# Optimization experiments

Hardware: AMD Instinct MI355X
Metric: run time of the kernel (lower is better)

The kernel has to match this reference:

```python
import jax, jax.numpy as jnp
import numpy as np

N_VOX = (128, 128, 8)            # (X, Y, Z) voxels
D_BINS = 66                      # int((50 - 0) / 0.75)
DEPTH_RANGE = (0.0, 50.0)
IMG_H, IMG_W = 512.0, 1408.0     # img_pad_shape / img_shape (features are stride-16: 32x88)
PC_RANGE = (-51.2, -51.2, -5.0, 51.2, 51.2, 3.0)


def _make_points():
    # voxel-center anchors, laid out so reshape(n_voxels[::-1]+[-1]) = [Z,Y,X,C] (x fastest)
    nx, ny, nz = N_VOX
    x0, y0, z0, x1, y1, z1 = PC_RANGE
    xc = x0 + (np.arange(nx) + 0.5) * (x1 - x0) / nx
    yc = y0 + (np.arange(ny) + 0.5) * (y1 - y0) / ny
    zc = z0 + (np.arange(nz) + 0.5) * (z1 - z0) / nz
    zz, yy, xx = np.meshgrid(zc, yc, xc, indexing='ij')
    return np.stack([xx, yy, zz], -1).reshape(-1, 3).astype(np.float32)


def _make_proj(B, N):
    # realistic ori_lidar2img: pinhole K @ [R|t], six surround cameras 60 deg apart
    K = np.array([[560., 0., 704., 0.], [0., 560., 256., 0.],
                  [0., 0., 1., 0.], [0., 0., 0., 1.]], np.float64)
    mats = []
    for n in range(N):
        th = 2.0 * np.pi * n / N
        fwd = np.array([np.cos(th), np.sin(th), 0.0])
        right = np.array([np.sin(th), -np.cos(th), 0.0])
        down = np.array([0.0, 0.0, -1.0])
        Rt = np.eye(4)
        Rt[:3, :3] = np.stack([right, down, fwd])
        Rt[:3, 3] = [0.0, 0.2, 0.0]
        mats.append(K @ Rt)
    P = np.stack(mats).astype(np.float32)
    return np.broadcast_to(P, (B, N, 4, 4)).copy()


def setup_inputs() -> dict:
    key = jax.random.key(0)
    B, N, C, H, W = 1, 6, 64, 32, 88
    k1, k2, k3 = jax.random.split(key, 3)
    return {
        'x_fov': jax.random.normal(k1, (B, N, C, H, W), jnp.float32),
        'w_dn': jax.random.normal(k2, (C + D_BINS, C), jnp.float32) * 0.05,
        'b_dn': jax.random.normal(k3, (C + D_BINS,), jnp.float32) * 0.05,
        'points': jnp.asarray(_make_points()),
        'proj_mats': jnp.asarray(_make_proj(B, N)),
    }


def _trilinear(vol, gx, gy, gz):
    # vol: [C, D, H, W]; gx/gy/gz: [P] continuous indices along W/H/D
    # grid_sample(align_corners=False, padding_mode='zeros') semantics
    C, D, H, W = vol.shape
    x0f, y0f, z0f = jnp.floor(gx), jnp.floor(gy), jnp.floor(gz)
    tx, ty, tz = gx - x0f, gy - y0f, gz - z0f
    x0, y0, z0 = x0f.astype(jnp.int32), y0f.astype(jnp.int32), z0f.astype(jnp.int32)
    out = jnp.zeros((C, gx.shape[0]), vol.dtype)
    for dz, wz in ((0, 1.0 - tz), (1, tz)):
        for dy, wy in ((0, 1.0 - ty), (1, ty)):
            for dx, wx in ((0, 1.0 - tx), (1, tx)):
                xi, yi, zi = x0 + dx, y0 + dy, z0 + dz
                inb = ((xi >= 0) & (xi < W) & (yi >= 0) & (yi < H)
                       & (zi >= 0) & (zi < D))
                w = (wx * wy * wz) * inb.astype(vol.dtype)  # [P]
                corner = vol[:, jnp.clip(zi, 0, D - 1),
                             jnp.clip(yi, 0, H - 1),
                             jnp.clip(xi, 0, W - 1)]        # [C, P]
                out = out + corner * w
    return out.T  # [P, C]


def reference(x_fov, w_dn, b_dn, points, proj_mats):
    B, N, C, H, W = x_fov.shape
    nx, ny, nz = N_VOX
    dr0, dr1 = DEPTH_RANGE
    # 1x1 conv depth_net
    y = jnp.einsum('bnchw,oc->bnohw', x_fov, w_dn) + b_dn[None, None, :, None, None]
    depth = jax.nn.softmax(y[:, :, :D_BINS], axis=2)       # [B,N,D,H,W]
    feat = y[:, :, D_BINS:]                                # [B,N,C,H,W]
    # LSS outer product -> [B,N,C,D,H,W]
    vol = depth[:, :, None] * feat[:, :, :, None]
    # project voxel centers into each camera
    hom = jnp.concatenate([points, jnp.ones_like(points[:, :1])], -1)  # [P,4]
    pts = jnp.einsum('bnij,pj->bnpi', proj_mats, hom)      # [B,N,P,4]
    z = pts[..., 2]
    zs = jnp.where(jnp.abs(z) > 1e-3, z, 1e-3)
    u = pts[..., 0] / zs
    v = pts[..., 1] / zs
    valid = ((u >= 0) & (u < IMG_W) & (v >= 0) & (v < IMG_H)
             & (z > dr0) & (z < dr1))                      # [B,N,P]
    # normalized->index coords (align_corners=False): idx = norm01*size - 0.5
    gx = u / IMG_W * W - 0.5
    gy = v / IMG_H * H - 0.5
    gz = (z - dr0) / (dr1 - dr0) * D_BINS - 0.5
    P = points.shape[0]
    samp = jax.vmap(_trilinear)(vol.reshape(B * N, C, D_BINS, H, W),
                                gx.reshape(B * N, P),
                                gy.reshape(B * N, P),
                                gz.reshape(B * N, P))      # [B*N,P,C]
    samp = samp.reshape(B, N, P, C) * valid[..., None].astype(samp.dtype)
    counts = valid.astype(samp.dtype).sum(1)               # [B,P]
    ssum = samp.sum(1)                                     # [B,P,C]
    out = jnp.where(counts[..., None] > 0,
                    ssum / jnp.clip(counts, 1e-3, None)[..., None],
                    jnp.zeros_like(ssum))
    # [B,P,C] -> [B,Z,Y,X,C] -> [B,C,X,Y,Z]
    return out.reshape(B, nz, ny, nx, C).transpose(0, 4, 3, 2, 1)
```

## Files before the change

kernel.cpp:

```cpp
#include <hip/hip_runtime.h>
#include <math.h>

#define NCAM 6
#define CCH  64
#define DB   66
#define FH   32
#define FW   88
#define NX   128
#define NY   128
#define NZ   8
#define NPTS (NX*NY*NZ)
#define NPIX (NCAM*FH*FW)
#define PPC  (FH*FW)

#define TPX   32
#define DN_T  256
#define WS2   132
#define YSS   35
#define OFF_XS 0
#define OFF_WT 2048
#define OFF_YS 2048
#define OFF_BS 10496
#define LDS_F  10626

__global__ __launch_bounds__(DN_T) void depthnet_kernel(
    const float* __restrict__ x_fov, const float* __restrict__ w_dn,
    const float* __restrict__ b_dn, float* __restrict__ feat_t,
    float* __restrict__ depth_t)
{
    __shared__ float lds[LDS_F];
    float* xs = lds + OFF_XS;
    float* wT = lds + OFF_WT;
    float* ys = lds + OFF_YS;
    float* bs = lds + OFF_BS;

    const int t   = threadIdx.x;
    const int T   = blockIdx.x * TPX;
    const int cam = T / PPC;
    const int ph0 = T - cam * PPC;

    if (t < DB + CCH) bs[t] = b_dn[t];
    for (int i = t; i < (DB + CCH) * CCH; i += DN_T) {
        const int o = i >> 6, c = i & 63;
        wT[c * WS2 + o] = w_dn[i];
    }
    {
        const float* xb = x_fov + (size_t)cam * CCH * PPC + ph0;
        const int c = t >> 2;
        const int q = t & 3;
        #pragma unroll
        for (int h = 0; h < 2; ++h) {
            const float4 v = *(const float4*)(xb + c * PPC + h * 16 + q * 4);
            *(float4*)(xs + c * TPX + h * 16 + q * 4) = v;
        }
    }
    __syncthreads();

    const int pq = t & 3;
    const int oq = t >> 2;
    float acc[2][8];
    float acc2[2][8];
    #pragma unroll
    for (int a = 0; a < 2; ++a)
        #pragma unroll
        for (int p = 0; p < 8; ++p) { acc[a][p] = 0.f; acc2[a][p] = 0.f; }

    {
        const float* xr  = xs + pq * 8;
        const float* wr  = wT + oq * 2;
        const float* wr2 = wT + 128;
        #pragma unroll 4
        for (int c = 0; c < 64; ++c) {
            const float4 xa = *(const float4*)(xr + c * TPX);
            const float4 xb2 = *(const float4*)(xr + c * TPX + 4);
            const float2 wv = *(const float2*)(wr + c * WS2);
            const float xv[8] = {xa.x, xa.y, xa.z, xa.w, xb2.x, xb2.y, xb2.z, xb2.w};
            #pragma unroll
            for (int p = 0; p < 8; ++p) {
                acc[0][p] += wv.x * xv[p];
                acc[1][p] += wv.y * xv[p];
            }
            if (oq == 0) {
                const float2 w2 = *(const float2*)(wr2 + c * WS2);
                #pragma unroll
                for (int p = 0; p < 8; ++p) {
                    acc2[0][p] += w2.x * xv[p];
                    acc2[1][p] += w2.y * xv[p];
                }
            }
        }
    }
    __syncthreads();

    #pragma unroll
    for (int a = 0; a < 2; ++a) {
        const int o = 2 * oq + a;
        const float b = bs[o];
        #pragma unroll
        for (int p = 0; p < 8; ++p) ys[o * YSS + pq * 8 + p] = acc[a][p] + b;
    }
    if (oq == 0) {
        #pragma unroll
        for (int a = 0; a < 2; ++a) {
            const int o = 128 + a;
            const float b = bs[o];
            #pragma unroll
            for (int p = 0; p < 8; ++p) ys[o * YSS + pq * 8 + p] = acc2[a][p] + b;
        }
    }
    __syncthreads();

    {
        const int spx = t >> 3;
        const int r   = t & 7;
        float m = -1e30f;
        #pragma unroll
        for (int i = 0; i < 9; ++i) {
            const int o = r + 8 * i;
            if (o < DB) m = fmaxf(m, ys[o * YSS + spx]);
        }
        m = fmaxf(m, __shfl_xor(m, 1));
        m = fmaxf(m, __shfl_xor(m, 2));
        m = fmaxf(m, __shfl_xor(m, 4));
        float e[9];
        float ssum = 0.f;
        #pragma unroll
        for (int i = 0; i < 9; ++i) {
            const int o = r + 8 * i;
            const float v = (o < DB) ? expf(ys[o * YSS + spx] - m) : 0.f;
            e[i] = v;
            ssum += v;
        }
        ssum += __shfl_xor(ssum, 1);
        ssum += __shfl_xor(ssum, 2);
        ssum += __shfl_xor(ssum, 4);
        const float inv = 1.f / ssum;
        #pragma unroll
        for (int i = 0; i < 9; ++i) {
            const int o = r + 8 * i;
            if (o < DB) depth_t[(size_t)(T + spx) * DB + o] = e[i] * inv;
        }
    }

    for (int i = t; i < TPX * CCH; i += DN_T) {
        const int px = i >> 6, o = i & 63;
        feat_t[(size_t)T * CCH + i] = ys[(DB + o) * YSS + px];
    }
}

__global__ __launch_bounds__(256) void splat_kernel(
    const float* __restrict__ feat_t, const float* __restrict__ depth_t,
    const float* __restrict__ proj, float* __restrict__ out)
{
    __shared__ float trans[64 * 33];
    const int t    = threadIdx.x;
    const int w    = t >> 6;
    const int lane = t & 63;
    const int g    = lane >> 3;
    const int s    = lane & 7;
    const int gb   = lane & 56;
    const int ix   = blockIdx.x >> 5;
    const int iy0  = 4 * (blockIdx.x & 31);
    const int iy   = iy0 + w;

    const double DXY = 102.4 / 128.0;
    const float px = (float)(-51.2 + (ix + 0.5) * DXY);
    const float py = (float)(-51.2 + (iy + 0.5) * DXY);
    const float pz = (float)(-5.0 + (g + 0.5) * 1.0);

    float wcs_l[4] = {0.f, 0.f, 0.f, 0.f};
    int   pixc_l[4] = {0, 0, 0, 0};
    bool validm = false;
    if (s < NCAM) {
        const float* M = proj + s * 16;
        const float u4 = M[0] * px + M[1] * py + M[2]  * pz + M[3];
        const float v4 = M[4] * px + M[5] * py + M[6]  * pz + M[7];
        const float z  = M[8] * px + M[9] * py + M[10] * pz + M[11];
        const float zs = fabsf(z) > 0.001f ? z : 0.001f;
        const float u = u4 / zs;
        const float v = v4 / zs;
        validm = (u >= 0.f) && (u < 1408.f) && (v >= 0.f) && (v < 512.f) &&
                 (z > 0.f) && (z < 50.f);
        if (validm) {
            const float gx = u / 1408.0f * (float)FW - 0.5f;
            const float gy = v / 512.0f  * (float)FH - 0.5f;
            const float gz = z / 50.0f   * (float)DB - 0.5f;
            const float xf = floorf(gx), yf = floorf(gy), zf = floorf(gz);
            const float tx = gx - xf, ty = gy - yf, tz = gz - zf;
            const int x0 = (int)xf, y0 = (int)yf, z0 = (int)zf;

            const float wz0 = (z0 >= 0 && z0 < DB) ? (1.f - tz) : 0.f;
            const float wz1 = (z0 + 1 < DB) ? tz : 0.f;
            const int zi0 = min(max(z0, 0), DB - 1);
            const int zi1 = min(max(z0 + 1, 0), DB - 1);

            #pragma unroll
            for (int dy = 0; dy < 2; ++dy) {
                const int yi = y0 + dy;
                const bool yin = (yi >= 0) & (yi < FH);
                const int yic = min(max(yi, 0), FH - 1);
                const float wy = (dy ? ty : 1.f - ty) * (yin ? 1.f : 0.f);
                #pragma unroll
                for (int dx = 0; dx < 2; ++dx) {
                    const int xi = x0 + dx;
                    const bool xin = (xi >= 0) & (xi < FW);
                    const int xic = min(max(xi, 0), FW - 1);
                    const float wx = (dx ? tx : 1.f - tx) * (xin ? 1.f : 0.f);
                    pixc_l[2 * dy + dx] = (s * FH + yic) * FW + xic;
                    wcs_l[2 * dy + dx]  = wx * wy;
                }
            }
            #pragma unroll
            for (int k = 0; k < 4; ++k) {
                const float* dptr = depth_t + (size_t)pixc_l[k] * DB;
                wcs_l[k] *= wz0 * dptr[zi0] + wz1 * dptr[zi1];
            }
        }
    }
    const unsigned long long bal = __ballot(validm);
    const float cnt = (float)__popcll((bal >> (g * 8)) & 0x3Full);

    float acc[8];
    #pragma unroll
    for (int a = 0; a < 8; ++a) acc[a] = 0.f;

    for (int cam = 0; cam < NCAM; ++cam) {
        if ((bal >> (gb + cam)) & 1ull) {
            #pragma unroll
            for (int k = 0; k < 4; ++k) {
                const float wc  = __shfl(wcs_l[k], gb | cam);
                const int   pcx = __shfl(pixc_l[k], gb | cam);
                const float* fb = feat_t + (size_t)pcx * CCH + s * 4;
                const float4 fa = *(const float4*)(fb);
                const float4 fh = *(const float4*)(fb + 32);
                acc[0] += wc * fa.x; acc[1] += wc * fa.y;
                acc[2] += wc * fa.z; acc[3] += wc * fa.w;
                acc[4] += wc * fh.x; acc[5] += wc * fh.y;
                acc[6] += wc * fh.z; acc[7] += wc * fh.w;
            }
        }
    }

    const float invc = cnt > 0.f ? 1.f / cnt : 0.f;
    #pragma unroll
    for (int j = 0; j < 4; ++j) {
        trans[(4 * s + j) * 33 + w * 8 + g]      = acc[j]     * invc;
        trans[(32 + 4 * s + j) * 33 + w * 8 + g] = acc[4 + j] * invc;
    }
    __syncthreads();
    {
        const int idx = t & 31;
        const int cb  = t >> 5;
        const size_t obase = (size_t)ix * (NY * NZ) + iy0 * 8 + idx;
        #pragma unroll
        for (int i = 0; i < 8; ++i) {
            const int c = cb + 8 * i;
            out[(size_t)c * NPTS + obase] = trans[c * 33 + idx];
        }
    }
}

extern "C" void kernel_launch(void* const* d_in, const int* in_sizes, int n_in,
                              void* d_out, int out_size, void* d_ws, size_t ws_size,
                              hipStream_t stream) {
    const float* x_fov = (const float*)d_in[0];
    const float* w_dn  = (const float*)d_in[1];
    const float* b_dn  = (const float*)d_in[2];
    const float* proj  = (const float*)d_in[4];
    float* out = (float*)d_out;

    float* feat_t  = (float*)d_ws;
    float* depth_t = feat_t + (size_t)NPIX * CCH;

    depthnet_kernel<<<NPIX / TPX, DN_T, 0, stream>>>(x_fov, w_dn, b_dn, feat_t, depth_t);

    splat_kernel<<<(NX * NY) / 4, 256, 0, stream>>>(feat_t, depth_t, proj, out);
}
```

Baseline: 102.5 us.

## Use one-wave splat blocks with swizzled block order and direct stores

The splat kernel now launches one 64-thread block per (x,y) column instead of four columns per 256-thread block. Blocks are remapped with a swizzle, (L&7)*2048 + (L>>3), which spreads consecutive block IDs across distant columns, presumably to balance work across XCDs and CUs. The LDS transpose and barrier are gone, and each thread writes its outputs straight to global memory. The cost is less coalesced stores: each warp now writes 8-float runs per channel instead of 32-float runs.

```diff
diff --git a/kernel.cpp b/kernel.cpp
--- a/kernel.cpp
+++ b/kernel.cpp
@@ -148,20 +148,18 @@
     }
 }
 
-__global__ __launch_bounds__(256) void splat_kernel(
+__global__ __launch_bounds__(64) void splat_kernel(
     const float* __restrict__ feat_t, const float* __restrict__ depth_t,
     const float* __restrict__ proj, float* __restrict__ out)
 {
-    __shared__ float trans[64 * 33];
-    const int t    = threadIdx.x;
-    const int w    = t >> 6;
-    const int lane = t & 63;
+    const int L  = blockIdx.x;
+    const int b  = (L & 7) * 2048 + (L >> 3);
+    const int ix = b >> 7;
+    const int iy = b & 127;
+    const int lane = threadIdx.x;
     const int g    = lane >> 3;
     const int s    = lane & 7;
     const int gb   = lane & 56;
-    const int ix   = blockIdx.x >> 5;
-    const int iy0  = 4 * (blockIdx.x & 31);
-    const int iy   = iy0 + w;
 
     const double DXY = 102.4 / 128.0;
     const float px = (float)(-51.2 + (ix + 0.5) * DXY);
@@ -242,21 +240,11 @@
     }
 
     const float invc = cnt > 0.f ? 1.f / cnt : 0.f;
+    const int obase = ix * (NY * NZ) + iy * NZ + g;
     #pragma unroll
     for (int j = 0; j < 4; ++j) {
-        trans[(4 * s + j) * 33 + w * 8 + g]      = acc[j]     * invc;
-        trans[(32 + 4 * s + j) * 33 + w * 8 + g] = acc[4 + j] * invc;
-    }
-    __syncthreads();
-    {
-        const int idx = t & 31;
-        const int cb  = t >> 5;
-        const size_t obase = (size_t)ix * (NY * NZ) + iy0 * 8 + idx;
-        #pragma unroll
-        for (int i = 0; i < 8; ++i) {
-            const int c = cb + 8 * i;
-            out[(size_t)c * NPTS + obase] = trans[c * 33 + idx];
-        }
+        out[(size_t)(4 * s + j) * NPTS + obase]      = acc[j]     * invc;
+        out[(size_t)(32 + 4 * s + j) * NPTS + obase] = acc[4 + j] * invc;
     }
 }
 
@@ -274,5 +262,5 @@
 
     depthnet_kernel<<<NPIX / TPX, DN_T, 0, stream>>>(x_fov, w_dn, b_dn, feat_t, depth_t);
 
-    splat_kernel<<<(NX * NY) / 4, 256, 0, stream>>>(feat_t, depth_t, proj, out);
+    splat_kernel<<<NX * NY, 64, 0, stream>>>(feat_t, depth_t, proj, out);
 }
```

Result: slower. 106.4 us (+3.8%).
